# Kernel tuning notes

Measured on AMD Instinct MI355X. Metric: run time of the kernel, lower is better.

The kernel has to match this reference:

```python
import jax, jax.numpy as jnp
import numpy as np

TAU_MIN, TAU_MAX = 1.5, 4.0
NUM_EXPERTS, TOP_K = 8, 2
V_TH = 1.0
BN_EPS = 1e-5
SG_ALPHA = 4.0  # spikingjelly Sigmoid surrogate default

@jax.custom_vjp
def spike(v):
    # Heaviside spike with sigmoid surrogate gradient
    return (v >= 0.0).astype(v.dtype)

def _spike_fwd(v):
    return spike(v), v

def _spike_bwd(v, g):
    s = jax.nn.sigmoid(SG_ALPHA * v)
    return (g * SG_ALPHA * s * (1.0 - s),)

spike.defvjp(_spike_fwd, _spike_bwd)

def lif(x, tau):
    # MultiStepLIFNode, v_reset=0 (hard reset), detach_reset=True. x: (T, ...)
    def step(v, xt):
        v = v + (xt - v) / tau          # charge
        s = spike(v - V_TH)             # fire
        v = v * (1.0 - jax.lax.stop_gradient(s))  # detached hard reset
        return v, s
    return jax.lax.scan(step, jnp.zeros_like(x[0]), x)[1]

def conv1x1(x, W, b):
    # x: (T,B,Cin,H,W), W: (Cout,Cin) -> (T,B,Cout,H,W)
    return jnp.einsum('tbchw,oc->tbohw', x, W) + b[None, None, :, None, None]

def bn_eval(x, scale, bias):
    # eval-mode BatchNorm2d with running_mean=0, running_var=1
    inv = scale / jnp.sqrt(1.0 + BN_EPS)
    return x * inv[None, None, :, None, None] + bias[None, None, :, None, None]

def expert_fwd(x, tau, W1, b1, s1, bb1, W2, b2, s2, bb2):
    # MS_MLP_Expert: LIF -> conv1x1 -> BN -> (+res) -> LIF -> conv1x1 -> BN -> (+res)
    identity = x
    h = lif(x, tau)
    h = bn_eval(conv1x1(h, W1, b1), s1, bb1)
    h = identity + h            # res: in_features == hidden_features
    identity = h
    o = lif(h, tau)
    o = bn_eval(conv1x1(o, W2, b2), s2, bb2)
    return o + identity

def moe_forward(x, router_W, router_b, router_bn_scale, router_bn_bias,
                W1, b1, bn1_scale, bn1_bias, W2, b2, bn2_scale, bn2_bias):
    T, B, C, H, W = x.shape
    taus = jnp.linspace(TAU_MIN, TAU_MAX, NUM_EXPERTS).astype(x.dtype)
    # --- SpikeRouter ---
    r = lif(x, 2.0)
    r = bn_eval(conv1x1(r, router_W, router_b), router_bn_scale, router_bn_bias)  # (T,B,E,H,W)
    logits_tb = r.mean(axis=(-2, -1))          # (T,B,E)
    # batch-level temporal routing: aggregate logits over T
    logits = logits_tb.mean(axis=0)            # (B,E)
    probs = jax.nn.softmax(logits, axis=-1)
    topw, topi = jax.lax.top_k(probs, TOP_K)   # (B,k)
    topw = topw / topw.sum(axis=-1, keepdims=True)
    dense_w = jnp.zeros((B, NUM_EXPERTS), dtype=x.dtype).at[
        jnp.arange(B)[:, None], topi].set(topw)  # (B,E)
    # --- experts: each processes the full temporal sequence ---
    ys = jax.vmap(expert_fwd, in_axes=(None, 0, 0, 0, 0, 0, 0, 0, 0, 0))(
        x, taus, W1, b1, bn1_scale, bn1_bias, W2, b2, bn2_scale, bn2_bias)  # (E,T,B,C,H,W)
    out = jnp.einsum('etbchw,be->tbchw', ys, dense_w)
    return out

def setup_inputs() -> dict:
    key = jax.random.key(0)
    ks = jax.random.split(key, 6)
    T, B, C, H, Wd = 4, 16, 384, 16, 16
    E = NUM_EXPERTS
    wscale = 1.0 / np.sqrt(C)
    return {
        'x': jax.random.normal(ks[0], (T, B, C, H, Wd), jnp.float32),
        'router_W': jax.random.normal(ks[1], (E, C), jnp.float32) * wscale,
        'router_b': jnp.zeros((E,), jnp.float32),
        'router_bn_scale': jnp.ones((E,), jnp.float32),
        'router_bn_bias': jnp.zeros((E,), jnp.float32),
        'W1': jax.random.normal(ks[2], (E, C, C), jnp.float32) * wscale,
        'b1': jnp.zeros((E, C), jnp.float32),
        'bn1_scale': jnp.ones((E, C), jnp.float32),
        'bn1_bias': jnp.zeros((E, C), jnp.float32),
        'W2': jax.random.normal(ks[3], (E, C, C), jnp.float32) * wscale,
        'b2': jnp.zeros((E, C), jnp.float32),
        'bn2_scale': jnp.ones((E, C), jnp.float32),
        'bn2_bias': jnp.zeros((E, C), jnp.float32),
    }

def reference(x, router_W, router_b, router_bn_scale, router_bn_bias,
              W1, b1, bn1_scale, bn1_bias, W2, b2, bn2_scale, bn2_bias):
    return moe_forward(x, router_W, router_b, router_bn_scale, router_bn_bias,
                       W1, b1, bn1_scale, bn1_bias, W2, b2, bn2_scale, bn2_bias)
```

## Files before the change

### kernel.cpp

```cpp
#include <hip/hip_runtime.h>
#include <math.h>

#define T_  4
#define B_  16
#define C_  384
#define HW_ 256
#define E_  8

typedef __attribute__((ext_vector_type(8))) __bf16 bf16x8;
typedef __attribute__((ext_vector_type(4))) float f32x4;

union FragU { uint4 u; bf16x8 v; };

__device__ __forceinline__ float tau_of(int e) {
    if (e == 7) return 4.0f;
    const float delta = 2.5f / 7.0f;
    return __fadd_rn(1.5f, __fmul_rn((float)e, delta));
}

__device__ __forceinline__ FragU expand_mask(unsigned m) {
    FragU f;
    f.u.x = ((m & 1u)   ? 0x3F80u : 0u) | ((m & 2u)   ? 0x3F800000u : 0u);
    f.u.y = ((m & 4u)   ? 0x3F80u : 0u) | ((m & 8u)   ? 0x3F800000u : 0u);
    f.u.z = ((m & 16u)  ? 0x3F80u : 0u) | ((m & 32u)  ? 0x3F800000u : 0u);
    f.u.w = ((m & 64u)  ? 0x3F80u : 0u) | ((m & 128u) ? 0x3F800000u : 0u);
    return f;
}

__global__ __launch_bounds__(256) void k_prep(const float* __restrict__ x,
        const float* __restrict__ W1, const float* __restrict__ W2,
        unsigned short* __restrict__ Whif, unsigned short* __restrict__ Wlof,
        float* __restrict__ m) {
    if (blockIdx.x < 1152) {
        int tid = blockIdx.x * 256 + threadIdx.x;
        int l = tid & 63;
        int f = tid >> 6;
        int osub = f % 24;
        int ksub = (f / 24) % 12;
        int cv = (f / 288) & 1;
        int e = f / 576;
        const float* Wsrc = (cv == 0 ? W1 : W2) + (size_t)e * C_ * C_;
        int o = osub * 16 + (l & 15);
        int c0 = ksub * 32 + (l >> 4) * 8;
        const float* src = Wsrc + (size_t)o * C_ + c0;
        unsigned hw[8], lw[8];
#pragma unroll
        for (int j = 0; j < 8; ++j) {
            float w = src[j];
            unsigned u = __float_as_uint(w);
            unsigned hi = (u + 0x7FFFu + ((u >> 16) & 1u)) >> 16;
            float hf = __uint_as_float(hi << 16);
            float res = __fsub_rn(w, hf);
            unsigned ru = __float_as_uint(res);
            unsigned lo = (ru + 0x7FFFu + ((ru >> 16) & 1u)) >> 16;
            hw[j] = hi & 0xFFFFu;
            lw[j] = lo & 0xFFFFu;
        }
        size_t dst = (size_t)f * 512 + (size_t)l * 8;
        uint4 hv = make_uint4(hw[0] | (hw[1] << 16), hw[2] | (hw[3] << 16),
                              hw[4] | (hw[5] << 16), hw[6] | (hw[7] << 16));
        uint4 lv = make_uint4(lw[0] | (lw[1] << 16), lw[2] | (lw[3] << 16),
                              lw[4] | (lw[5] << 16), lw[6] | (lw[7] << 16));
        *reinterpret_cast<uint4*>(Whif + dst) = hv;
        *reinterpret_cast<uint4*>(Wlof + dst) = lv;
    } else {
        int bc = blockIdx.x - 1152;
        int b = bc / C_, c = bc % C_;
        int p = threadIdx.x;
        int wv = threadIdx.x >> 6;
        __shared__ int cnt[T_][4];
        float v = 0.0f;
#pragma unroll
        for (int t = 0; t < T_; ++t) {
            float xv = x[((t * B_ + b) * C_ + c) * HW_ + p];
            v = __fadd_rn(v, __fdiv_rn(__fsub_rn(xv, v), 2.0f));
            bool s = (__fsub_rn(v, 1.0f) >= 0.0f);
            if (s) v = 0.0f;
            unsigned long long mask = __ballot(s);
            if ((threadIdx.x & 63) == 0) cnt[t][wv] = (int)__popcll(mask);
        }
        __syncthreads();
        if (threadIdx.x < T_) {
            int t = threadIdx.x;
            int tot = cnt[t][0] + cnt[t][1] + cnt[t][2] + cnt[t][3];
            m[(t * B_ + b) * C_ + c] = (float)tot * 0.00390625f;
        }
    }
}

__device__ __forceinline__ void conv_mfma(const unsigned short* __restrict__ Whif,
                                          const unsigned short* __restrict__ Wlof,
                                          unsigned base,
                                          const unsigned char* __restrict__ sm,
                                          f32x4 (&acc)[3][4],
                                          int wave, int lane, int q, int pl) {
    const unsigned lane8 = (unsigned)lane * 8u;
    const unsigned wbase = base + (unsigned)(wave * 3) * 512u + lane8;
    FragU c0f, c1f, c2f, n0f, n1f, n2f;
    c0f.u = *reinterpret_cast<const uint4*>(Wlof + wbase);
    c1f.u = *reinterpret_cast<const uint4*>(Wlof + wbase + 512u);
    c2f.u = *reinterpret_cast<const uint4*>(Wlof + wbase + 1024u);
#pragma unroll 1
    for (int ksub = 0; ksub < 12; ++ksub) {
        unsigned fo = wbase + (unsigned)ksub * 24u * 512u;
        FragU bf[T_];
#pragma unroll
        for (int t = 0; t < T_; ++t) {
            unsigned mbyte = sm[(t * 16 + pl) * 48 + ksub * 4 + q];
            bf[t] = expand_mask(mbyte);
        }
        n0f.u = *reinterpret_cast<const uint4*>(Whif + fo);
        n1f.u = *reinterpret_cast<const uint4*>(Whif + fo + 512u);
        n2f.u = *reinterpret_cast<const uint4*>(Whif + fo + 1024u);
#pragma unroll
        for (int t = 0; t < T_; ++t) {
            acc[0][t] = __builtin_amdgcn_mfma_f32_16x16x32_bf16(c0f.v, bf[t].v, acc[0][t], 0, 0, 0);
            acc[1][t] = __builtin_amdgcn_mfma_f32_16x16x32_bf16(c1f.v, bf[t].v, acc[1][t], 0, 0, 0);
            acc[2][t] = __builtin_amdgcn_mfma_f32_16x16x32_bf16(c2f.v, bf[t].v, acc[2][t], 0, 0, 0);
        }
        if (ksub < 11) {
            unsigned fn = fo + 24u * 512u;
            c0f.u = *reinterpret_cast<const uint4*>(Wlof + fn);
            c1f.u = *reinterpret_cast<const uint4*>(Wlof + fn + 512u);
            c2f.u = *reinterpret_cast<const uint4*>(Wlof + fn + 1024u);
        }
#pragma unroll
        for (int t = 0; t < T_; ++t) {
            acc[0][t] = __builtin_amdgcn_mfma_f32_16x16x32_bf16(n0f.v, bf[t].v, acc[0][t], 0, 0, 0);
            acc[1][t] = __builtin_amdgcn_mfma_f32_16x16x32_bf16(n1f.v, bf[t].v, acc[1][t], 0, 0, 0);
            acc[2][t] = __builtin_amdgcn_mfma_f32_16x16x32_bf16(n2f.v, bf[t].v, acc[2][t], 0, 0, 0);
        }
    }
}

__global__ __launch_bounds__(512, 2) void k_expert(
        const float* __restrict__ x, const float* __restrict__ m,
        const float* __restrict__ rW, const float* __restrict__ rb,
        const float* __restrict__ rbs, const float* __restrict__ rbb,
        const unsigned short* __restrict__ Whif, const unsigned short* __restrict__ Wlof,
        const float* __restrict__ b1, const float* __restrict__ s1sc, const float* __restrict__ s1bi,
        const float* __restrict__ b2, const float* __restrict__ s2sc, const float* __restrict__ s2bi,
        float* __restrict__ out) {
    int blk = blockIdx.x;
    int b = (blk & 7) | (((blk >> 3) & 1) << 3);
    int ptile = blk >> 4;

    __shared__ unsigned char s1m[2][T_ * 16 * 48];
    __shared__ unsigned char s2m[2][T_ * 16 * 48];
    __shared__ float bns[2 * 6 * C_];
    __shared__ float lg[E_];
    __shared__ float wsl[2];
    __shared__ int esl[2];

    int tid = threadIdx.x;
    int wave = tid >> 6;
    int lane = tid & 63;
    int q = lane >> 4;
    int pl = lane & 15;
    int p = ptile * 16 + pl;
    float denom = sqrtf(__fadd_rn(1.0f, 1e-5f));

    if (tid < 64) {
        int combo = tid & 31, half = tid >> 5;
        int e = combo >> 2, t = combo & 3;
        float dot = 0.0f;
        int c0 = half * 192;
        for (int c = 0; c < 192; ++c)
            dot = fmaf(rW[e * C_ + c0 + c], m[(t * B_ + b) * C_ + c0 + c], dot);
        dot += __shfl_down(dot, 32);
        float Ar = __fdiv_rn(rbs[e], denom);
        float lt = __fadd_rn(__fmul_rn(__fadd_rn(dot, rb[e]), Ar), rbb[e]);
        lt = __fadd_rn(lt, __shfl_xor(lt, 1));
        lt = __fadd_rn(lt, __shfl_xor(lt, 2));
        if (half == 0 && t == 0) lg[e] = __fmul_rn(lt, 0.25f);
    }
    __syncthreads();
    if (tid == 0) {
        float pr[E_];
        float mx = lg[0];
        for (int i = 1; i < E_; ++i) mx = fmaxf(mx, lg[i]);
        float s = 0.0f;
        for (int i = 0; i < E_; ++i) { pr[i] = expf(__fsub_rn(lg[i], mx)); s = __fadd_rn(s, pr[i]); }
        for (int i = 0; i < E_; ++i) pr[i] = __fdiv_rn(pr[i], s);
        int i0 = 0;
        for (int i = 1; i < E_; ++i) if (pr[i] > pr[i0]) i0 = i;
        int i1 = (i0 == 0) ? 1 : 0;
        for (int i = 0; i < E_; ++i) if (i != i0 && pr[i] > pr[i1]) i1 = i;
        float s2 = __fadd_rn(pr[i0], pr[i1]);
        wsl[0] = __fdiv_rn(pr[i0], s2);
        wsl[1] = __fdiv_rn(pr[i1], s2);
        esl[0] = i0;
        esl[1] = i1;
    }
    __syncthreads();

    int e0 = esl[0], e1 = esl[1];
    float tau0 = tau_of(e0), tau1 = tau_of(e1);

    if (tid < C_) {
#pragma unroll
        for (int r_ = 0; r_ < 2; ++r_) {
            int er = (r_ == 0) ? e0 : e1;
            bns[(r_ * 6 + 0) * C_ + tid] = __fdiv_rn(s1sc[er * C_ + tid], denom);
            bns[(r_ * 6 + 1) * C_ + tid] = b1[er * C_ + tid];
            bns[(r_ * 6 + 2) * C_ + tid] = s1bi[er * C_ + tid];
            bns[(r_ * 6 + 3) * C_ + tid] = __fdiv_rn(s2sc[er * C_ + tid], denom);
            bns[(r_ * 6 + 4) * C_ + tid] = b2[er * C_ + tid];
            bns[(r_ * 6 + 5) * C_ + tid] = s2bi[er * C_ + tid];
        }
    }

#pragma unroll 1
    for (int task = tid; task < 48 * 16; task += 512) {
        int cb = task >> 4;
        int tpl = task & 15;
        int tp = ptile * 16 + tpl;
        float va[8], vb[8];
#pragma unroll
        for (int j = 0; j < 8; ++j) { va[j] = 0.0f; vb[j] = 0.0f; }
#pragma unroll
        for (int t = 0; t < T_; ++t) {
            int gbase = ((t * B_ + b) * C_ + cb * 8) * HW_ + tp;
            unsigned mb0 = 0, mb1 = 0;
#pragma unroll
            for (int j = 0; j < 8; ++j) {
                float xv = x[gbase + j * HW_];
                va[j] = __fadd_rn(va[j], __fdiv_rn(__fsub_rn(xv, va[j]), tau0));
                if (__fsub_rn(va[j], 1.0f) >= 0.0f) { mb0 |= (1u << j); va[j] = 0.0f; }
                vb[j] = __fadd_rn(vb[j], __fdiv_rn(__fsub_rn(xv, vb[j]), tau1));
                if (__fsub_rn(vb[j], 1.0f) >= 0.0f) { mb1 |= (1u << j); vb[j] = 0.0f; }
            }
            s1m[0][(t * 16 + tpl) * 48 + cb] = (unsigned char)mb0;
            s1m[1][(t * 16 + tpl) * 48 + cb] = (unsigned char)mb1;
        }
    }
    __syncthreads();

    float part[3][4][4];
#pragma unroll
    for (int os = 0; os < 3; ++os)
#pragma unroll
        for (int t = 0; t < T_; ++t)
#pragma unroll
            for (int r = 0; r < 4; ++r) part[os][t][r] = 0.0f;

#pragma unroll 1
    for (int r_ = 0; r_ < 2; ++r_) {
        int er = (r_ == 0) ? e0 : e1;
        float wr = wsl[r_];
        float taur = (r_ == 0) ? tau0 : tau1;
        unsigned base1 = (unsigned)(er * 2) * 12u * 24u * 512u;

        f32x4 acc[3][4];
#pragma unroll
        for (int os = 0; os < 3; ++os)
#pragma unroll
            for (int t = 0; t < T_; ++t) acc[os][t] = (f32x4)0.0f;

        conv_mfma(Whif, Wlof, base1, &s1m[r_][0], acc, wave, lane, q, pl);

#pragma unroll
        for (int os = 0; os < 3; ++os) {
            float v2s[4] = {0.f, 0.f, 0.f, 0.f};
#pragma unroll
            for (int t = 0; t < T_; ++t) {
                unsigned nb = 0;
#pragma unroll
                for (int r = 0; r < 4; ++r) {
                    int o = wave * 48 + os * 16 + q * 4 + r;
                    int gi = ((t * B_ + b) * C_ + o) * HW_ + p;
                    float y = acc[os][t][r];
                    float h = __fadd_rn(x[gi],
                        __fadd_rn(__fmul_rn(__fadd_rn(y, bns[(r_ * 6 + 1) * C_ + o]),
                                            bns[(r_ * 6 + 0) * C_ + o]),
                                  bns[(r_ * 6 + 2) * C_ + o]));
                    part[os][t][r] = fmaf(wr, h, part[os][t][r]);
                    v2s[r] = __fadd_rn(v2s[r], __fdiv_rn(__fsub_rn(h, v2s[r]), taur));
                    if (__fsub_rn(v2s[r], 1.0f) >= 0.0f) { nb |= (1u << r); v2s[r] = 0.f; }
                }
                unsigned nb_hi = (unsigned)__shfl_down((int)nb, 16);
                if ((q & 1) == 0) {
                    int cbyte = wave * 6 + os * 2 + (q >> 1);
                    s2m[r_][(t * 16 + pl) * 48 + cbyte] = (unsigned char)(nb | (nb_hi << 4));
                }
            }
        }
    }
    __syncthreads();

#pragma unroll 1
    for (int r_ = 0; r_ < 2; ++r_) {
        int er = (r_ == 0) ? e0 : e1;
        float wr = wsl[r_];
        unsigned base2 = (unsigned)(er * 2 + 1) * 12u * 24u * 512u;

        f32x4 acc[3][4];
#pragma unroll
        for (int os = 0; os < 3; ++os)
#pragma unroll
            for (int t = 0; t < T_; ++t) acc[os][t] = (f32x4)0.0f;

        conv_mfma(Whif, Wlof, base2, &s2m[r_][0], acc, wave, lane, q, pl);

#pragma unroll
        for (int os = 0; os < 3; ++os)
#pragma unroll
            for (int t = 0; t < T_; ++t)
#pragma unroll
                for (int r = 0; r < 4; ++r) {
                    int o = wave * 48 + os * 16 + q * 4 + r;
                    float y = acc[os][t][r];
                    float val = __fadd_rn(__fmul_rn(__fadd_rn(y, bns[(r_ * 6 + 4) * C_ + o]),
                                                    bns[(r_ * 6 + 3) * C_ + o]),
                                          bns[(r_ * 6 + 5) * C_ + o]);
                    part[os][t][r] = fmaf(wr, val, part[os][t][r]);
                }
    }

#pragma unroll
    for (int os = 0; os < 3; ++os)
#pragma unroll
        for (int t = 0; t < T_; ++t)
#pragma unroll
            for (int r = 0; r < 4; ++r) {
                int o = wave * 48 + os * 16 + q * 4 + r;
                int gi = ((t * B_ + b) * C_ + o) * HW_ + p;
                out[gi] = part[os][t][r];
            }
}

extern "C" void kernel_launch(void* const* d_in, const int* in_sizes, int n_in,
                              void* d_out, int out_size, void* d_ws, size_t ws_size,
                              hipStream_t stream) {
    const float* x    = (const float*)d_in[0];
    const float* rW   = (const float*)d_in[1];
    const float* rb   = (const float*)d_in[2];
    const float* rbs  = (const float*)d_in[3];
    const float* rbb  = (const float*)d_in[4];
    const float* W1   = (const float*)d_in[5];
    const float* b1   = (const float*)d_in[6];
    const float* s1sc = (const float*)d_in[7];
    const float* s1bi = (const float*)d_in[8];
    const float* W2   = (const float*)d_in[9];
    const float* b2   = (const float*)d_in[10];
    const float* s2sc = (const float*)d_in[11];
    const float* s2bi = (const float*)d_in[12];
    float* out = (float*)d_out;

    unsigned short* Whif = (unsigned short*)d_ws;
    unsigned short* Wlof = Whif + 2359296;
    float* m = (float*)((char*)d_ws + 9437184);

    hipLaunchKernelGGL(k_prep, dim3(1152 + B_ * C_), dim3(256), 0, stream,
                       x, W1, W2, Whif, Wlof, m);
    hipLaunchKernelGGL(k_expert, dim3(256), dim3(512), 0, stream,
                       x, m, rW, rb, rbs, rbb, Whif, Wlof,
                       b1, s1sc, s1bi, b2, s2sc, s2bi, out);
}
```

Before: 164.0 us.

## Run the two routed experts concurrently in separate 512-thread teams

Doubles the block to 1024 threads so each half computes one of the two top-k experts in parallel, instead of looping over them one after another. The second team's weighted partial sums are staged in a new LDS buffer of about 100 KB. Team 0 writes its first-stage contribution straight to global output, then after a barrier re-reads it and adds its own second stage plus the LDS partials. This doubles the waves per CU, but it tightens the register budget through the launch bounds, adds extra global output traffic and a large LDS footprint, and changes the floating-point summation order.

```diff
diff --git a/kernel.cpp b/kernel.cpp
--- a/kernel.cpp
+++ b/kernel.cpp
@@ -93,9 +93,9 @@
                                           unsigned base,
                                           const unsigned char* __restrict__ sm,
                                           f32x4 (&acc)[3][4],
-                                          int wave, int lane, int q, int pl) {
+                                          int tw, int lane, int q, int pl) {
     const unsigned lane8 = (unsigned)lane * 8u;
-    const unsigned wbase = base + (unsigned)(wave * 3) * 512u + lane8;
+    const unsigned wbase = base + (unsigned)(tw * 3) * 512u + lane8;
     FragU c0f, c1f, c2f, n0f, n1f, n2f;
     c0f.u = *reinterpret_cast<const uint4*>(Wlof + wbase);
     c1f.u = *reinterpret_cast<const uint4*>(Wlof + wbase + 512u);
@@ -133,7 +133,7 @@
     }
 }
 
-__global__ __launch_bounds__(512, 2) void k_expert(
+__global__ __launch_bounds__(1024, 4) void k_expert(
         const float* __restrict__ x, const float* __restrict__ m,
         const float* __restrict__ rW, const float* __restrict__ rb,
         const float* __restrict__ rbs, const float* __restrict__ rbb,
@@ -148,12 +148,15 @@
     __shared__ unsigned char s1m[2][T_ * 16 * 48];
     __shared__ unsigned char s2m[2][T_ * 16 * 48];
     __shared__ float bns[2 * 6 * C_];
+    __shared__ float lds_part[512 * 49];
     __shared__ float lg[E_];
     __shared__ float wsl[2];
     __shared__ int esl[2];
 
     int tid = threadIdx.x;
-    int wave = tid >> 6;
+    int team = tid >> 9;
+    int tid2 = tid & 511;
+    int tw = tid2 >> 6;
     int lane = tid & 63;
     int q = lane >> 4;
     int pl = lane & 15;
@@ -194,70 +197,56 @@
     }
     __syncthreads();
 
-    int e0 = esl[0], e1 = esl[1];
-    float tau0 = tau_of(e0), tau1 = tau_of(e1);
-
-    if (tid < C_) {
-#pragma unroll
-        for (int r_ = 0; r_ < 2; ++r_) {
-            int er = (r_ == 0) ? e0 : e1;
-            bns[(r_ * 6 + 0) * C_ + tid] = __fdiv_rn(s1sc[er * C_ + tid], denom);
-            bns[(r_ * 6 + 1) * C_ + tid] = b1[er * C_ + tid];
-            bns[(r_ * 6 + 2) * C_ + tid] = s1bi[er * C_ + tid];
-            bns[(r_ * 6 + 3) * C_ + tid] = __fdiv_rn(s2sc[er * C_ + tid], denom);
-            bns[(r_ * 6 + 4) * C_ + tid] = b2[er * C_ + tid];
-            bns[(r_ * 6 + 5) * C_ + tid] = s2bi[er * C_ + tid];
-        }
+    int er = esl[team];
+    float wgt = wsl[team];
+    float tau = tau_of(er);
+
+    if (tid < 2 * C_) {
+        int r_ = tid / C_;
+        int o = tid % C_;
+        int eo = esl[r_] * C_ + o;
+        bns[(r_ * 6 + 0) * C_ + o] = __fdiv_rn(s1sc[eo], denom);
+        bns[(r_ * 6 + 1) * C_ + o] = b1[eo];
+        bns[(r_ * 6 + 2) * C_ + o] = s1bi[eo];
+        bns[(r_ * 6 + 3) * C_ + o] = __fdiv_rn(s2sc[eo], denom);
+        bns[(r_ * 6 + 4) * C_ + o] = b2[eo];
+        bns[(r_ * 6 + 5) * C_ + o] = s2bi[eo];
     }
 
 #pragma unroll 1
-    for (int task = tid; task < 48 * 16; task += 512) {
+    for (int task = tid2; task < 48 * 16; task += 512) {
         int cb = task >> 4;
         int tpl = task & 15;
         int tp = ptile * 16 + tpl;
-        float va[8], vb[8];
-#pragma unroll
-        for (int j = 0; j < 8; ++j) { va[j] = 0.0f; vb[j] = 0.0f; }
+        float v[8];
+#pragma unroll
+        for (int j = 0; j < 8; ++j) v[j] = 0.0f;
 #pragma unroll
         for (int t = 0; t < T_; ++t) {
             int gbase = ((t * B_ + b) * C_ + cb * 8) * HW_ + tp;
-            unsigned mb0 = 0, mb1 = 0;
+            unsigned mb = 0;
 #pragma unroll
             for (int j = 0; j < 8; ++j) {
                 float xv = x[gbase + j * HW_];
-                va[j] = __fadd_rn(va[j], __fdiv_rn(__fsub_rn(xv, va[j]), tau0));
-                if (__fsub_rn(va[j], 1.0f) >= 0.0f) { mb0 |= (1u << j); va[j] = 0.0f; }
-                vb[j] = __fadd_rn(vb[j], __fdiv_rn(__fsub_rn(xv, vb[j]), tau1));
-                if (__fsub_rn(vb[j], 1.0f) >= 0.0f) { mb1 |= (1u << j); vb[j] = 0.0f; }
+                v[j] = __fadd_rn(v[j], __fdiv_rn(__fsub_rn(xv, v[j]), tau));
+                if (__fsub_rn(v[j], 1.0f) >= 0.0f) { mb |= (1u << j); v[j] = 0.0f; }
             }
-            s1m[0][(t * 16 + tpl) * 48 + cb] = (unsigned char)mb0;
-            s1m[1][(t * 16 + tpl) * 48 + cb] = (unsigned char)mb1;
+            s1m[team][(t * 16 + tpl) * 48 + cb] = (unsigned char)mb;
         }
     }
     __syncthreads();
 
-    float part[3][4][4];
-#pragma unroll
-    for (int os = 0; os < 3; ++os)
-#pragma unroll
-        for (int t = 0; t < T_; ++t)
-#pragma unroll
-            for (int r = 0; r < 4; ++r) part[os][t][r] = 0.0f;
-
-#pragma unroll 1
-    for (int r_ = 0; r_ < 2; ++r_) {
-        int er = (r_ == 0) ? e0 : e1;
-        float wr = wsl[r_];
-        float taur = (r_ == 0) ? tau0 : tau1;
-        unsigned base1 = (unsigned)(er * 2) * 12u * 24u * 512u;
-
+    const unsigned base1 = (unsigned)(er * 2) * 12u * 24u * 512u;
+    const unsigned base2 = (unsigned)(er * 2 + 1) * 12u * 24u * 512u;
+
+    {
         f32x4 acc[3][4];
 #pragma unroll
         for (int os = 0; os < 3; ++os)
 #pragma unroll
             for (int t = 0; t < T_; ++t) acc[os][t] = (f32x4)0.0f;
 
-        conv_mfma(Whif, Wlof, base1, &s1m[r_][0], acc, wave, lane, q, pl);
+        conv_mfma(Whif, Wlof, base1, &s1m[team][0], acc, tw, lane, q, pl);
 
 #pragma unroll
         for (int os = 0; os < 3; ++os) {
@@ -267,40 +256,37 @@
                 unsigned nb = 0;
 #pragma unroll
                 for (int r = 0; r < 4; ++r) {
-                    int o = wave * 48 + os * 16 + q * 4 + r;
+                    int o = tw * 48 + os * 16 + q * 4 + r;
                     int gi = ((t * B_ + b) * C_ + o) * HW_ + p;
                     float y = acc[os][t][r];
                     float h = __fadd_rn(x[gi],
-                        __fadd_rn(__fmul_rn(__fadd_rn(y, bns[(r_ * 6 + 1) * C_ + o]),
-                                            bns[(r_ * 6 + 0) * C_ + o]),
-                                  bns[(r_ * 6 + 2) * C_ + o]));
-                    part[os][t][r] = fmaf(wr, h, part[os][t][r]);
-                    v2s[r] = __fadd_rn(v2s[r], __fdiv_rn(__fsub_rn(h, v2s[r]), taur));
+                        __fadd_rn(__fmul_rn(__fadd_rn(y, bns[(team * 6 + 1) * C_ + o]),
+                                            bns[(team * 6 + 0) * C_ + o]),
+                                  bns[(team * 6 + 2) * C_ + o]));
+                    float contrib = __fmul_rn(wgt, h);
+                    if (team == 0) out[gi] = contrib;
+                    else lds_part[tid2 * 49 + os * 16 + t * 4 + r] = contrib;
+                    v2s[r] = __fadd_rn(v2s[r], __fdiv_rn(__fsub_rn(h, v2s[r]), tau));
                     if (__fsub_rn(v2s[r], 1.0f) >= 0.0f) { nb |= (1u << r); v2s[r] = 0.f; }
                 }
                 unsigned nb_hi = (unsigned)__shfl_down((int)nb, 16);
                 if ((q & 1) == 0) {
-                    int cbyte = wave * 6 + os * 2 + (q >> 1);
-                    s2m[r_][(t * 16 + pl) * 48 + cbyte] = (unsigned char)(nb | (nb_hi << 4));
+                    int cbyte = tw * 6 + os * 2 + (q >> 1);
+                    s2m[team][(t * 16 + pl) * 48 + cbyte] = (unsigned char)(nb | (nb_hi << 4));
                 }
             }
         }
     }
     __syncthreads();
 
-#pragma unroll 1
-    for (int r_ = 0; r_ < 2; ++r_) {
-        int er = (r_ == 0) ? e0 : e1;
-        float wr = wsl[r_];
-        unsigned base2 = (unsigned)(er * 2 + 1) * 12u * 24u * 512u;
-
+    {
         f32x4 acc[3][4];
 #pragma unroll
         for (int os = 0; os < 3; ++os)
 #pragma unroll
             for (int t = 0; t < T_; ++t) acc[os][t] = (f32x4)0.0f;
 
-        conv_mfma(Whif, Wlof, base2, &s2m[r_][0], acc, wave, lane, q, pl);
+        conv_mfma(Whif, Wlof, base2, &s2m[team][0], acc, tw, lane, q, pl);
 
 #pragma unroll
         for (int os = 0; os < 3; ++os)
@@ -308,25 +294,35 @@
             for (int t = 0; t < T_; ++t)
 #pragma unroll
                 for (int r = 0; r < 4; ++r) {
-                    int o = wave * 48 + os * 16 + q * 4 + r;
+                    int o = tw * 48 + os * 16 + q * 4 + r;
                     float y = acc[os][t][r];
-                    float val = __fadd_rn(__fmul_rn(__fadd_rn(y, bns[(r_ * 6 + 4) * C_ + o]),
-                                                    bns[(r_ * 6 + 3) * C_ + o]),
-                                          bns[(r_ * 6 + 5) * C_ + o]);
-                    part[os][t][r] = fmaf(wr, val, part[os][t][r]);
+                    float val = __fmul_rn(wgt,
+                        __fadd_rn(__fmul_rn(__fadd_rn(y, bns[(team * 6 + 4) * C_ + o]),
+                                            bns[(team * 6 + 3) * C_ + o]),
+                                  bns[(team * 6 + 5) * C_ + o]));
+                    if (team == 1) {
+                        int li = tid2 * 49 + os * 16 + t * 4 + r;
+                        lds_part[li] = __fadd_rn(lds_part[li], val);
+                    } else {
+                        acc[os][t][r] = val;
+                    }
                 }
-    }
-
-#pragma unroll
-    for (int os = 0; os < 3; ++os)
-#pragma unroll
-        for (int t = 0; t < T_; ++t)
-#pragma unroll
-            for (int r = 0; r < 4; ++r) {
-                int o = wave * 48 + os * 16 + q * 4 + r;
-                int gi = ((t * B_ + b) * C_ + o) * HW_ + p;
-                out[gi] = part[os][t][r];
-            }
+        __syncthreads();
+
+        if (team == 0) {
+#pragma unroll
+            for (int os = 0; os < 3; ++os)
+#pragma unroll
+                for (int t = 0; t < T_; ++t)
+#pragma unroll
+                    for (int r = 0; r < 4; ++r) {
+                        int o = tw * 48 + os * 16 + q * 4 + r;
+                        int gi = ((t * B_ + b) * C_ + o) * HW_ + p;
+                        float pp = lds_part[tid2 * 49 + os * 16 + t * 4 + r];
+                        out[gi] = __fadd_rn(__fadd_rn(out[gi], acc[os][t][r]), pp);
+                    }
+        }
+    }
 }
 
 extern "C" void kernel_launch(void* const* d_in, const int* in_sizes, int n_in,
@@ -353,7 +349,7 @@
 
     hipLaunchKernelGGL(k_prep, dim3(1152 + B_ * C_), dim3(256), 0, stream,
                        x, W1, W2, Whif, Wlof, m);
-    hipLaunchKernelGGL(k_expert, dim3(256), dim3(512), 0, stream,
+    hipLaunchKernelGGL(k_expert, dim3(256), dim3(1024), 0, stream,
                        x, m, rW, rb, rbs, rbb, Whif, Wlof,
                        b1, s1sc, s1bi, b2, s2sc, s2bi, out);
 }
```

Result: slower. 182.0 us (+10.9%).
